# Kernel optimization log

Measured on AMD Instinct MI355X. Metric: run time of the kernel, lower is better.

The kernel has to match this reference:

```python
import jax, jax.numpy as jnp
import numpy as np

# Hyperparameters from init_kwargs
K = 1024           # num_embeddings
D = 256            # embedding_dim
COMMIT = 0.25      # commitment_cost
DECAY = 0.99
LAMBDA = 1e-05
NU = 0.1
TAU = 0.5


def setup_inputs() -> dict:
    key = jax.random.key(0)
    k1, k2, k3 = jax.random.split(key, 3)
    B, H, W = 32, 32, 32
    N = B * H * W
    inputs = jax.random.normal(k1, (B, D, H, W), jnp.float32)
    weight = jax.random.normal(k2, (K, D), jnp.float32) * 0.02  # codebook
    # EMA buffers as initialized on first training step (non-kmeans branch)
    ema_count = jnp.full((K,), N / K, jnp.float32)
    ema_weight = weight * ema_count[:, None]
    # Gumbel noise used by F.gumbel_softmax(-distances, tau, hard=True)
    gumbel_noise = jax.random.gumbel(k3, (N, K), jnp.float32)
    return {"inputs": inputs, "weight": weight, "ema_count": ema_count,
            "ema_weight": ema_weight, "gumbel_noise": gumbel_noise}


def reference(inputs, weight, ema_count, ema_weight, gumbel_noise):
    B, C, H, W = inputs.shape
    # b d h w -> (b h w) d
    x = jnp.transpose(inputs, (0, 2, 3, 1)).reshape(-1, C)  # [N, D]
    N = x.shape[0]

    distances = (jnp.sum(x * x, axis=1, keepdims=True)
                 + jnp.sum(weight * weight, axis=1)
                 - 2.0 * jnp.einsum('nd,kd->nk', x, weight))

    soft_encodings = jax.nn.softmax(-distances / TAU, axis=-1)  # [N, K]

    # Hard gumbel-softmax sample (computed under no_grad in torch):
    # argmax((logits + g)/tau) == argmax(logits + g), logits = -distances
    idx = jnp.argmax(-distances + gumbel_noise, axis=-1)        # [N]
    encodings = jax.nn.one_hot(idx, K, dtype=x.dtype)           # [N, K]

    quantized = (encodings @ weight).reshape(B, H, W, C)        # [B,H,W,D]

    # EMA codebook update (training branch, no_grad)
    new_count = ema_count * DECAY + jnp.sum(soft_encodings, axis=0) * (1.0 - DECAY)
    new_count = (new_count + LAMBDA) / (N + K * LAMBDA) * N
    d_weight = jnp.einsum('nk,nd->kd', soft_encodings, x)
    new_ema_weight = ema_weight * DECAY + d_weight * (1.0 - DECAY)
    new_embedding = new_ema_weight / new_count[:, None]

    # Negative-entropy commitment loss on soft assignments
    probs = soft_encodings
    loss_latents = jnp.mean(jnp.sum(probs * jnp.log(jnp.clip(probs, 1e-08)), axis=-1))
    loss = COMMIT * loss_latents

    # quantized + nu*(quantized - detach(quantized)) == quantized in value
    quantized = quantized + NU * (quantized - jax.lax.stop_gradient(quantized))

    avg_probs = jnp.mean(encodings, axis=0)
    perplexity = jnp.exp(-jnp.sum(avg_probs * jnp.log(avg_probs + 1e-10)))

    quantized_out = jnp.transpose(quantized, (0, 3, 1, 2))  # [B,D,H,W]
    return (loss, quantized_out, perplexity, encodings,
            new_count, new_ema_weight, new_embedding)
```

## Files before the change

### kernel.cpp

```cpp
#include <hip/hip_runtime.h>
#include <math.h>

#define NROWS 32768
#define KCB   1024
#define DDIM  256
#define NHALF 16384

#define O_LOSS 0
#define O_Q    1
#define O_PERP 8388609
#define O_ENC  8388610
#define O_NCNT 41943042
#define O_EMAW 41944066
#define O_EMB  42206210

#define E_XS3   2
#define E_S     12582914

#define W_WSQ  0
#define W_XSQ  1024
#define W_IDX  33792
#define W_COL  66560
#define W_HCNT 67584
#define W_BENT 68608
#define W_T2I  77824
#define W_WB   143360
#define W_MROW 274432
#define W_IROW 307200

typedef __attribute__((ext_vector_type(8))) short bf16x8;
typedef __attribute__((ext_vector_type(4))) float f32x4;

#define GLOAD_LDS16(g, l) __builtin_amdgcn_global_load_lds( \
    (const __attribute__((address_space(1))) unsigned int*)(g), \
    (__attribute__((address_space(3))) unsigned int*)(l), 16, 0, 0)

__device__ __forceinline__ float wred_sum(float v) {
#pragma unroll
  for (int off = 32; off > 0; off >>= 1) v += __shfl_xor(v, off);
  return v;
}
__device__ __forceinline__ ushort f2bf(float f) {
  union { float f; unsigned u; } c; c.f = f;
  unsigned u = c.u;
  return (ushort)((u + 0x7fffu + ((u >> 16) & 1u)) >> 16);
}
__device__ __forceinline__ float bf2f(ushort h) {
  union { unsigned u; float f; } c; c.u = ((unsigned)h) << 16;
  return c.f;
}

__global__ void k_init(float* __restrict__ hcnt, float* __restrict__ colsum) {
  int i = blockIdx.x * 256 + threadIdx.x;
  if (i < 1024) { hcnt[i] = 0.f; colsum[i] = 0.f; }
}

__global__ void k_wsplit(const float* __restrict__ w, float* __restrict__ wsq,
                         ushort* __restrict__ WB) {
  int t = threadIdx.x;
  int lane = t & 63, wv = t >> 6;
  int k = blockIdx.x * 4 + wv;
  int d0 = lane * 4;
  float4 v = *(const float4*)&w[(size_t)k * DDIM + d0];
  float s = v.x * v.x + v.y * v.y + v.z * v.z + v.w * v.w;
  s = wred_sum(s);
  if (lane == 0) wsq[k] = s;
  float vv[4] = {v.x, v.y, v.z, v.w};
  union { ushort u[4]; uint2 q; } hh;
#pragma unroll
  for (int q = 0; q < 4; ++q) hh.u[q] = f2bf(vv[q]);
  *(uint2*)&WB[(size_t)k * 256 + d0] = hh.q;
}

__global__ __launch_bounds__(256) void k_xsplit(const float* __restrict__ x,
                                                ushort* __restrict__ XS3,
                                                float* __restrict__ xsq) {
  __shared__ __align__(16) ushort sl[32 * 776];
  __shared__ float sq[32 * 9];
  int t = threadIdx.x;
  int b = blockIdx.x >> 5, mt = blockIdx.x & 31;
  int m0 = mt * 32, mloc = t & 31, dgrp = t >> 5;
  const float* xb = x + (size_t)b * DDIM * 1024 + m0 + mloc;
  float s = 0.f;
#pragma unroll
  for (int jj = 0; jj < 8; ++jj) {
    int d0 = dgrp * 32 + jj * 4;
    float vv[4];
#pragma unroll
    for (int q = 0; q < 4; ++q) vv[q] = xb[(size_t)(d0 + q) * 1024];
    union { ushort u[4]; uint2 q; } hh, mi, lo;
#pragma unroll
    for (int q = 0; q < 4; ++q) {
      float v = vv[q];
      ushort h = f2bf(v);
      float r1 = v - bf2f(h);
      ushort m_ = f2bf(r1);
      float r2 = r1 - bf2f(m_);
      hh.u[q] = h; mi.u[q] = m_; lo.u[q] = f2bf(r2);
      s = fmaf(v, v, s);
    }
    int base = mloc * 776;
    *(uint2*)&sl[base + d0] = hh.q;
    *(uint2*)&sl[base + 256 + d0] = mi.q;
    *(uint2*)&sl[base + 512 + d0] = lo.q;
  }
  sq[mloc * 9 + dgrp] = s;
  __syncthreads();
  if (t < 32) {
    float ss = 0.f;
#pragma unroll
    for (int gq = 0; gq < 8; ++gq) ss += sq[t * 9 + gq];
    xsq[b * 1024 + m0 + t] = ss;
  }
  ushort* dst = XS3 + (size_t)(b * 1024 + m0) * 768;
#pragma unroll
  for (int p = 0; p < 12; ++p) {
    int idx = p * 256 + t;
    int row = idx / 96;
    int co = idx - row * 96;
    *(uint4*)&dst[(size_t)row * 768 + co * 8] = *(uint4*)&sl[row * 776 + co * 8];
  }
}

__global__ __launch_bounds__(256) void k_gemm1t(const ushort* __restrict__ XS3h,
                                                const ushort* __restrict__ WB,
                                                const float* __restrict__ wsq,
                                                const float* __restrict__ xsqh,
                                                float* __restrict__ S) {
  __shared__ __align__(16) ushort Asl[2][8192];
  __shared__ __align__(16) ushort Bsl[2][8192];
  __shared__ float xsl[128];
  __shared__ float wsl[128];
  int t = threadIdx.x;
  int h = blockIdx.x;
  int xcd = h & 7, seq = h >> 3;
  int kt = seq & 7;
  int nt = xcd * 16 + (seq >> 3);
  int n0 = nt * 128;
  int k0 = kt * 128;
  int l = t & 63, wid = t >> 6;
  int wr = wid >> 1, wc = wid & 1;
  int hi = l >> 4, c = l & 15;

  if (t < 128) { xsl[t] = xsqh[n0 + t]; wsl[t] = wsq[k0 + t]; }

  f32x4 zero = {0.f, 0.f, 0.f, 0.f};
  f32x4 acc[4][4];
#pragma unroll
  for (int i = 0; i < 4; ++i)
#pragma unroll
    for (int j = 0; j < 4; ++j) acc[i][j] = zero;

  const char* XSb = (const char*)XS3h;
  const char* WBb = (const char*)WB;
  int lr = l >> 3;
  int lsw = ((l & 7) ^ lr) << 4;

#define STAGE(s_, b_)                                                              \
  {                                                                                \
    size_t bofs_ = (size_t)((s_) & 3) << 7;                                        \
    size_t aofs_ = ((s_) < 4) ? ((size_t)(s_) << 7)                                \
                              : (size_t)(512 + (((s_) - 4) << 7));                 \
    char* Ad_ = (char*)Asl + (b_) * 16384;                                         \
    char* Bd_ = (char*)Bsl + (b_) * 16384;                                         \
    _Pragma("unroll")                                                              \
    for (int q_ = 0; q_ < 4; ++q_) {                                               \
      int seg_ = wid * 32 + q_ * 8;                                                \
      GLOAD_LDS16(XSb + (size_t)(n0 + seg_ + lr) * 1536 + aofs_ + lsw,             \
                  Ad_ + seg_ * 128);                                               \
      GLOAD_LDS16(WBb + (size_t)(k0 + seg_ + lr) * 512 + bofs_ + lsw,              \
                  Bd_ + seg_ * 128);                                               \
    }                                                                              \
  }

  STAGE(0, 0);
  asm volatile("s_waitcnt vmcnt(0)" ::: "memory");
  __builtin_amdgcn_s_barrier();
  __builtin_amdgcn_sched_barrier(0);

  int buf = 0;
  for (int s = 0; s < 8; ++s) {
    if (s < 7) STAGE(s + 1, buf ^ 1);
    const ushort* Ab = &Asl[buf][0];
    const ushort* Bb = &Bsl[buf][0];
#pragma unroll
    for (int kk = 0; kk < 2; ++kk) {
      bf16x8 af[4], bg[4];
#pragma unroll
      for (int i = 0; i < 4; ++i) {
        int row = wr * 64 + i * 16 + c;
        int ch = (kk * 4 + hi) ^ (row & 7);
        af[i] = *(const bf16x8*)&Ab[row * 64 + ch * 8];
      }
#pragma unroll
      for (int j = 0; j < 4; ++j) {
        int row = wc * 64 + j * 16 + c;
        int ch = (kk * 4 + hi) ^ (row & 7);
        bg[j] = *(const bf16x8*)&Bb[row * 64 + ch * 8];
      }
#pragma unroll
      for (int i = 0; i < 4; ++i)
#pragma unroll
        for (int j = 0; j < 4; ++j)
          acc[i][j] = __builtin_amdgcn_mfma_f32_16x16x32_bf16(af[i], bg[j], acc[i][j], 0, 0, 0);
    }
    asm volatile("s_waitcnt vmcnt(0)" ::: "memory");
    __builtin_amdgcn_s_barrier();
    buf ^= 1;
  }
#undef STAGE

#pragma unroll
  for (int i = 0; i < 4; ++i) {
#pragma unroll
    for (int r = 0; r < 4; ++r) {
      int nl = wr * 64 + i * 16 + hi * 4 + r;
      float xs = xsl[nl];
#pragma unroll
      for (int j = 0; j < 4; ++j) {
        int kl = wc * 64 + j * 16 + c;
        float nd = fmaf(2.f, acc[i][j][r], -(xs + wsl[kl]));
        S[(size_t)(n0 + nl) * 1024 + k0 + kl] = nd;
      }
    }
  }
}

__global__ __launch_bounds__(512) void k_rowfuse(const float* __restrict__ S,
                                                 const float* __restrict__ Gh,
                                                 float* __restrict__ benth,
                                                 int* __restrict__ t2igh,
                                                 ushort* __restrict__ sTp) {
  __shared__ ushort lds[64 * 65];
  __shared__ float Ml[64], Il[64];
  __shared__ float went[8];
  int t = threadIdx.x;
  int l = t & 63, wv = t >> 6;
  int n0 = blockIdx.x * 64;
  float entacc = 0.f;
  for (int it = 0; it < 8; ++it) {
    int nloc = wv * 8 + it;
    int n = n0 + nloc;
    const float* row = S + ((size_t)n << 10);
    const float* grow = Gh + ((size_t)n << 10);
    float v[16];
    float mx = -3.0e38f;
    float v1 = -3.0e38f, v2 = -3.0e38f;
    int i1 = 0x7fffffff, i2 = 0x7fffffff;
#pragma unroll
    for (int j = 0; j < 4; ++j) {
      float4 a = *(const float4*)&row[j * 256 + l * 4];
      float4 gg = *(const float4*)&grow[j * 256 + l * 4];
      float av[4] = {a.x, a.y, a.z, a.w};
      float gv[4] = {gg.x, gg.y, gg.z, gg.w};
#pragma unroll
      for (int q = 0; q < 4; ++q) {
        v[j * 4 + q] = av[q];
        mx = fmaxf(mx, av[q]);
        float sc = av[q] + gv[q];
        int kk = j * 256 + l * 4 + q;
        if (sc > v1 || (sc == v1 && kk < i1)) { v2 = v1; i2 = i1; v1 = sc; i1 = kk; }
        else if (sc > v2 || (sc == v2 && kk < i2)) { v2 = sc; i2 = kk; }
      }
    }
#pragma unroll
    for (int off = 1; off < 64; off <<= 1) {
      mx = fmaxf(mx, __shfl_xor(mx, off));
      float ov1 = __shfl_xor(v1, off), ov2 = __shfl_xor(v2, off);
      int oi1 = __shfl_xor(i1, off), oi2 = __shfl_xor(i2, off);
      bool fB = (ov1 > v1) || (ov1 == v1 && oi1 < i1);
      float nv1 = fB ? ov1 : v1; int ni1 = fB ? oi1 : i1;
      float ca = fB ? v1 : ov1;  int cia = fB ? i1 : oi1;
      float cb = fB ? ov2 : v2;  int cib = fB ? oi2 : i2;
      bool sB = (cb > ca) || (cb == ca && cib < cia);
      v1 = nv1; i1 = ni1;
      v2 = sB ? cb : ca; i2 = sB ? cib : cia;
    }
    float M = 2.f * mx;
    float e[16]; float ps = 0.f;
#pragma unroll
    for (int u = 0; u < 16; ++u) { e[u] = __expf(fmaf(2.f, v[u], -M)); ps += e[u]; }
    ps = wred_sum(ps);
    float inv = 1.f / ps;
    float ent = 0.f;
#pragma unroll
    for (int u = 0; u < 16; ++u) {
      float sfv = e[u] * inv;
      ent += sfv * __logf(fmaxf(sfv, 1e-8f));
    }
    ent = wred_sum(ent);
    entacc += ent;
    if (l == 0) {
      t2igh[n * 2] = i1; t2igh[n * 2 + 1] = i2;
      Ml[nloc] = M; Il[nloc] = inv;
    }
  }
  if (l == 0) went[wv] = entacc;
  __syncthreads();
  if (t == 0) {
    float s = 0.f;
#pragma unroll
    for (int q = 0; q < 8; ++q) s += went[q];
    benth[blockIdx.x] = s;
  }
  int row2 = t >> 3, c8 = (t & 7) * 8;
  float M2 = Ml[row2], inv2 = Il[row2];
  for (int kt = 0; kt < 16; ++kt) {
    int k0 = kt * 64;
    const float* sp = &S[(size_t)(n0 + row2) * 1024 + k0 + c8];
    float4 a = *(const float4*)sp;
    float4 b = *(const float4*)(sp + 4);
    float sv[8] = {a.x, a.y, a.z, a.w, b.x, b.y, b.z, b.w};
    ushort* d = &lds[row2 * 65 + c8];
#pragma unroll
    for (int j = 0; j < 8; ++j)
      d[j] = f2bf(__expf(fmaf(2.f, sv[j], -M2)) * inv2);
    __syncthreads();
    int krow = t >> 3, nc8 = (t & 7) * 8;
    uint* dst = (uint*)&sTp[(size_t)(k0 + krow) * NHALF + n0 + nc8];
#pragma unroll
    for (int j = 0; j < 4; ++j) {
      uint lo = lds[(nc8 + 2 * j) * 65 + krow];
      uint hh = lds[(nc8 + 2 * j + 1) * 65 + krow];
      dst[j] = lo | (hh << 16);
    }
    __syncthreads();
  }
}

__global__ __launch_bounds__(256) void k_rowstat(const float* __restrict__ S,
                                                 const float* __restrict__ Gh,
                                                 float* __restrict__ Mrowh,
                                                 float* __restrict__ Irowh,
                                                 float* __restrict__ benth,
                                                 int* __restrict__ t2igh) {
  __shared__ float went[4];
  int t = threadIdx.x;
  int l = t & 63, wv = t >> 6;
  int n = blockIdx.x * 4 + wv;
  const float* row = S + ((size_t)n << 10);
  const float* grow = Gh + ((size_t)n << 10);
  float v[16];
  float mx = -3.0e38f;
  float v1 = -3.0e38f, v2 = -3.0e38f;
  int i1 = 0x7fffffff, i2 = 0x7fffffff;
#pragma unroll
  for (int j = 0; j < 4; ++j) {
    float4 a = *(const float4*)&row[j * 256 + l * 4];
    float4 gg = *(const float4*)&grow[j * 256 + l * 4];
    float av[4] = {a.x, a.y, a.z, a.w};
    float gv[4] = {gg.x, gg.y, gg.z, gg.w};
#pragma unroll
    for (int q = 0; q < 4; ++q) {
      v[j * 4 + q] = av[q];
      mx = fmaxf(mx, av[q]);
      float sc = av[q] + gv[q];
      int kk = j * 256 + l * 4 + q;
      if (sc > v1 || (sc == v1 && kk < i1)) { v2 = v1; i2 = i1; v1 = sc; i1 = kk; }
      else if (sc > v2 || (sc == v2 && kk < i2)) { v2 = sc; i2 = kk; }
    }
  }
#pragma unroll
  for (int off = 1; off < 64; off <<= 1) {
    mx = fmaxf(mx, __shfl_xor(mx, off));
    float ov1 = __shfl_xor(v1, off), ov2 = __shfl_xor(v2, off);
    int oi1 = __shfl_xor(i1, off), oi2 = __shfl_xor(i2, off);
    bool fB = (ov1 > v1) || (ov1 == v1 && oi1 < i1);
    float nv1 = fB ? ov1 : v1; int ni1 = fB ? oi1 : i1;
    float ca = fB ? v1 : ov1;  int cia = fB ? i1 : oi1;
    float cb = fB ? ov2 : v2;  int cib = fB ? oi2 : i2;
    bool sB = (cb > ca) || (cb == ca && cib < cia);
    v1 = nv1; i1 = ni1;
    v2 = sB ? cb : ca; i2 = sB ? cib : cia;
  }
  float M = 2.f * mx;
  float e[16]; float ps = 0.f;
#pragma unroll
  for (int u = 0; u < 16; ++u) { e[u] = __expf(fmaf(2.f, v[u], -M)); ps += e[u]; }
  ps = wred_sum(ps);
  float inv = 1.f / ps;
  float ent = 0.f;
#pragma unroll
  for (int u = 0; u < 16; ++u) {
    float sfv = e[u] * inv;
    ent += sfv * __logf(fmaxf(sfv, 1e-8f));
  }
  ent = wred_sum(ent);
  if (l == 0) {
    t2igh[n * 2] = i1; t2igh[n * 2 + 1] = i2;
    Mrowh[n] = M; Irowh[n] = inv;
    went[wv] = ent;
  }
  __syncthreads();
  if (t == 0) benth[blockIdx.x] = went[0] + went[1] + went[2] + went[3];
}

__global__ __launch_bounds__(512) void k_rowwrite(const float* __restrict__ S,
                                                  const float* __restrict__ Mrowh,
                                                  const float* __restrict__ Irowh,
                                                  ushort* __restrict__ sTp) {
  __shared__ ushort lds[64 * 65];
  __shared__ float Ml[64], Il[64];
  int t = threadIdx.x;
  int n0 = blockIdx.x * 64;
  if (t < 64) { Ml[t] = Mrowh[n0 + t]; Il[t] = Irowh[n0 + t]; }
  __syncthreads();
  for (int kt = 0; kt < 16; ++kt) {
    int k0 = kt * 64;
    int row = t >> 3, c8 = (t & 7) * 8;
    float M = Ml[row], inv = Il[row];
    const float* sp = &S[(size_t)(n0 + row) * 1024 + k0 + c8];
    float4 a = *(const float4*)sp;
    float4 b = *(const float4*)(sp + 4);
    float sv[8] = {a.x, a.y, a.z, a.w, b.x, b.y, b.z, b.w};
    ushort* d = &lds[row * 65 + c8];
#pragma unroll
    for (int j = 0; j < 8; ++j)
      d[j] = f2bf(__expf(fmaf(2.f, sv[j], -M)) * inv);
    __syncthreads();
    int krow = t >> 3, nc8 = (t & 7) * 8;
    uint* dst = (uint*)&sTp[(size_t)(k0 + krow) * NHALF + n0 + nc8];
#pragma unroll
    for (int j = 0; j < 4; ++j) {
      uint lo = lds[(nc8 + 2 * j) * 65 + krow];
      uint hh = lds[(nc8 + 2 * j + 1) * 65 + krow];
      dst[j] = lo | (hh << 16);
    }
    __syncthreads();
  }
}

__global__ __launch_bounds__(256) void k_refine(const ushort* __restrict__ XS3,
                                                const float* __restrict__ w,
                                                const float* __restrict__ wsq,
                                                const float* __restrict__ xsq,
                                                const float* __restrict__ G,
                                                const int* __restrict__ t2ig,
                                                int* __restrict__ idxArr,
                                                float* __restrict__ hcnt) {
  int t = threadIdx.x;
  int l = t & 63, wv = t >> 6;
  int base = blockIdx.x * 64 + wv * 16;
  int d0 = l * 4;
  for (int rr = 0; rr < 16; ++rr) {
    int n = base + rr;
    const ushort* p = XS3 + (size_t)n * 768;
    union { uint2 q; ushort u[4]; } ha, ma, la;
    ha.q = *(const uint2*)&p[d0];
    ma.q = *(const uint2*)&p[256 + d0];
    la.q = *(const uint2*)&p[512 + d0];
    float xv[4];
#pragma unroll
    for (int q = 0; q < 4; ++q) xv[q] = bf2f(ha.u[q]) + bf2f(ma.u[q]) + bf2f(la.u[q]);
    float xs = xsq[n];
    int ia = t2ig[n * 2], ib = t2ig[n * 2 + 1];
    float sc[2];
    int ids[2] = {ia, ib};
#pragma unroll
    for (int cdd = 0; cdd < 2; ++cdd) {
      int id = ids[cdd];
      const float* wr = w + (size_t)id * DDIM;
      float4 wv4 = *(const float4*)&wr[d0];
      float d = xv[0] * wv4.x + xv[1] * wv4.y + xv[2] * wv4.z + xv[3] * wv4.w;
      d = wred_sum(d);
      sc[cdd] = fmaf(2.f, d, -xs) - wsq[id] + G[((size_t)n << 10) + id];
    }
    int win = (sc[1] > sc[0] || (sc[1] == sc[0] && ib < ia)) ? ib : ia;
    if (l == 0) {
      idxArr[n] = win;
      atomicAdd(&hcnt[win], 1.f);
    }
  }
}

__global__ void k_quant(const float* __restrict__ w, const int* __restrict__ idxArr,
                        float* __restrict__ outQ) {
  int n = blockIdx.x * 256 + threadIdx.x;
  int b = n >> 10, m = n & 1023;
  int id = idxArr[n];
  const float* wr = w + (size_t)id * DDIM;
  float* o = outQ + (size_t)b * DDIM * 1024 + m;
#pragma unroll 4
  for (int d = 0; d < DDIM; ++d) o[(size_t)d * 1024] = wr[d];
}

__global__ __launch_bounds__(512) void k_gemm2_mfma(const ushort* __restrict__ sT0,
                                                    const ushort* __restrict__ sT1,
                                                    const float* __restrict__ x,
                                                    ushort* __restrict__ P,
                                                    float* __restrict__ colsum) {
  __shared__ __align__(16) ushort Abuf[256 * 72];
  __shared__ __align__(16) ushort Bbuf[128 * 72];
  int t = threadIdx.x;
  int h = blockIdx.x;
  int xcd = h & 7, seq = h >> 3;
  int ns = xcd * 4 + (seq >> 3);
  int ktdt = seq & 7;
  int kt = ktdt & 3, dt = ktdt >> 2;
  int k0 = kt * 256, d0 = dt * 128;
  int l = t & 63, wv = t >> 6;
  int wk = wv >> 1, wd = wv & 1;
  const ushort* Abase = (ns < 16) ? sT0 : sT1;
  size_t nloc0 = (size_t)(ns & 15) * 1024;
  f32x4 zero = {0.f, 0.f, 0.f, 0.f};
  f32x4 acc[4][4];
#pragma unroll
  for (int i = 0; i < 4; ++i)
#pragma unroll
    for (int j = 0; j < 4; ++j) acc[i][j] = zero;
  float colacc[4] = {0.f, 0.f, 0.f, 0.f};

  int colv = (t & 7) * 8;
  int rbase = t >> 3;
  for (int s = 0; s < 16; ++s) {
#pragma unroll
    for (int p = 0; p < 4; ++p) {
      int row = p * 64 + rbase;
      const uint* ap = (const uint*)(Abase + (size_t)(k0 + row) * NHALF + nloc0 + s * 64 + colv);
      uint4 v; v.x = ap[0]; v.y = ap[1]; v.z = ap[2]; v.w = ap[3];
      *(uint4*)&Abuf[row * 72 + colv] = v;
    }
#pragma unroll
    for (int p = 0; p < 2; ++p) {
      int row = p * 64 + rbase;
      const float* xp = &x[((size_t)ns * DDIM + d0 + row) * 1024 + s * 64 + colv];
      float4 a = *(const float4*)xp;
      float4 b = *(const float4*)(xp + 4);
      union { ushort u[8]; uint4 q; } pk;
      pk.u[0] = f2bf(a.x); pk.u[1] = f2bf(a.y); pk.u[2] = f2bf(a.z); pk.u[3] = f2bf(a.w);
      pk.u[4] = f2bf(b.x); pk.u[5] = f2bf(b.y); pk.u[6] = f2bf(b.z); pk.u[7] = f2bf(b.w);
      *(uint4*)&Bbuf[row * 72 + colv] = pk.q;
    }
    __syncthreads();
    bf16x8 af[4], bfr[4];
#pragma unroll
    for (int nb2 = 0; nb2 < 2; ++nb2) {
#pragma unroll
      for (int sub = 0; sub < 4; ++sub) {
        af[sub] = *(const bf16x8*)&Abuf[(wk * 64 + sub * 16 + (l & 15)) * 72 + nb2 * 32 + (l >> 4) * 8];
        bfr[sub] = *(const bf16x8*)&Bbuf[(wd * 64 + sub * 16 + (l & 15)) * 72 + nb2 * 32 + (l >> 4) * 8];
      }
      if (dt == 0 && wd == 0) {
#pragma unroll
        for (int sub = 0; sub < 4; ++sub)
#pragma unroll
          for (int q = 0; q < 8; ++q)
            colacc[sub] += bf2f((ushort)af[sub][q]);
      }
#pragma unroll
      for (int i = 0; i < 4; ++i)
#pragma unroll
        for (int j = 0; j < 4; ++j)
          acc[i][j] = __builtin_amdgcn_mfma_f32_16x16x32_bf16(af[i], bfr[j], acc[i][j], 0, 0, 0);
    }
    __syncthreads();
  }
  ushort* Pb = P + (size_t)ns * (KCB * DDIM);
#pragma unroll
  for (int i = 0; i < 4; ++i)
#pragma unroll
    for (int j = 0; j < 4; ++j) {
#pragma unroll
      for (int r = 0; r < 4; ++r) {
        int k = k0 + wk * 64 + i * 16 + (l >> 4) * 4 + r;
        int d = d0 + wd * 64 + j * 16 + (l & 15);
        Pb[(size_t)k * DDIM + d] = f2bf(acc[i][j][r]);
      }
    }
  if (dt == 0 && wd == 0) {
#pragma unroll
    for (int sub = 0; sub < 4; ++sub) {
      float s = colacc[sub];
      s += __shfl_xor(s, 16);
      s += __shfl_xor(s, 32);
      if (l < 16) atomicAdd(&colsum[k0 + wk * 64 + sub * 16 + l], s);
    }
  }
}

__global__ void k_final1(const float* __restrict__ hcnt, const float* __restrict__ bent,
                         float* __restrict__ out) {
  __shared__ float red[1024];
  int t = threadIdx.x;
  float s = 0.f;
  for (int i = t; i < 4352; i += 1024) s += bent[i];
  red[t] = s;
  __syncthreads();
  for (int off = 512; off > 0; off >>= 1) { if (t < off) red[t] += red[t + off]; __syncthreads(); }
  if (t == 0) out[O_LOSS] = 0.25f * (red[0] / 32768.0f);
  __syncthreads();
  float avg = hcnt[t] * (1.0f / 32768.0f);
  red[t] = avg * logf(avg + 1e-10f);
  __syncthreads();
  for (int off = 512; off > 0; off >>= 1) { if (t < off) red[t] += red[t + off]; __syncthreads(); }
  if (t == 0) out[O_PERP] = expf(-red[0]);
}

__global__ void k_reduce_final2(const ushort* __restrict__ P,
                                const float* __restrict__ ema_w,
                                const float* __restrict__ ema_count,
                                const float* __restrict__ colsum,
                                float* __restrict__ outNC,
                                float* __restrict__ outEW,
                                float* __restrict__ outEMB) {
  int i4 = (blockIdx.x * 256 + threadIdx.x) * 4;
  int k = i4 >> 8;
  float nc = ema_count[k] * 0.99f + colsum[k] * 0.01f;
  nc = (nc + 1e-5f) / (32768.0f + 1024.0f * 1e-5f) * 32768.0f;
  if ((i4 & 255) == 0) outNC[k] = nc;
  float s0 = 0.f, s1 = 0.f, s2 = 0.f, s3 = 0.f;
#pragma unroll
  for (int ns = 0; ns < 32; ++ns) {
    uint2 v = *(const uint2*)&P[(size_t)ns * (KCB * DDIM) + i4];
    s0 += bf2f((ushort)(v.x & 0xffffu)); s1 += bf2f((ushort)(v.x >> 16));
    s2 += bf2f((ushort)(v.y & 0xffffu)); s3 += bf2f((ushort)(v.y >> 16));
  }
  float4 ew4 = *(const float4*)&ema_w[i4];
  float invnc = 1.0f / nc;
  float e0 = ew4.x * 0.99f + s0 * 0.01f;
  float e1 = ew4.y * 0.99f + s1 * 0.01f;
  float e2 = ew4.z * 0.99f + s2 * 0.01f;
  float e3 = ew4.w * 0.99f + s3 * 0.01f;
  float4 ewo = {e0, e1, e2, e3};
  float4 emo = {e0 * invnc, e1 * invnc, e2 * invnc, e3 * invnc};
  *(float4*)&outEW[i4] = ewo;
  *(float4*)&outEMB[i4] = emo;
}

__global__ void k_onehot(const int* __restrict__ idxArr, float* __restrict__ E) {
  int gid = blockIdx.x * 256 + threadIdx.x;
  int n = gid >> 8;
  int k4 = (gid & 255) * 4;
  int id = idxArr[n];
  float2* E2 = (float2*)E;
  size_t base = ((size_t)n * KCB + k4) >> 1;
  float2 vA = {(float)(k4 == id), (float)(k4 + 1 == id)};
  float2 vB = {(float)(k4 + 2 == id), (float)(k4 + 3 == id)};
  E2[base] = vA;
  E2[base + 1] = vB;
}

extern "C" void kernel_launch(void* const* d_in, const int* in_sizes, int n_in,
                              void* d_out, int out_size, void* d_ws, size_t ws_size,
                              hipStream_t stream) {
  const float* x = (const float*)d_in[0];
  const float* w = (const float*)d_in[1];
  const float* ema_count = (const float*)d_in[2];
  const float* ema_w = (const float*)d_in[3];
  const float* g = (const float*)d_in[4];
  float* out = (float*)d_out;
  float* ws = (float*)d_ws;

  float* wsq    = ws + W_WSQ;
  float* xsq    = ws + W_XSQ;
  int*   idxArr = (int*)(ws + W_IDX);
  float* colsum = ws + W_COL;
  float* hcnt   = ws + W_HCNT;
  float* bent   = ws + W_BENT;
  int*   top2i  = (int*)(ws + W_T2I);
  ushort* WB    = (ushort*)(ws + W_WB);
  float* Mrow   = ws + W_MROW;
  float* Irow   = ws + W_IROW;

  float* outQ = out + O_Q;
  float* outE = out + O_ENC;

  ushort* XS3    = (ushort*)(outE + E_XS3);
  float*  Sslot  = outE + E_S;
  ushort* Pbf    = (ushort*)Sslot;
  ushort* softT1 = (ushort*)(outE + E_XS3);
  ushort* softT0 = (ushort*)outQ;

  k_init<<<4, 256, 0, stream>>>(hcnt, colsum);
  k_wsplit<<<256, 256, 0, stream>>>(w, wsq, WB);
  k_xsplit<<<1024, 256, 0, stream>>>(x, XS3, xsq);
  k_gemm1t<<<1024, 256, 0, stream>>>(XS3, WB, wsq, xsq, Sslot);
  k_rowfuse<<<256, 512, 0, stream>>>(Sslot, g, bent, top2i, softT0);
  k_gemm1t<<<1024, 256, 0, stream>>>(XS3 + (size_t)NHALF * 768, WB,
                                     wsq, xsq + NHALF, Sslot);
  k_rowstat<<<4096, 256, 0, stream>>>(Sslot, g + (size_t)NHALF * 1024,
                                      Mrow, Irow, bent + 256, top2i + NHALF * 2);
  k_refine<<<512, 256, 0, stream>>>(XS3, w, wsq, xsq, g, top2i, idxArr, hcnt);
  k_rowwrite<<<256, 512, 0, stream>>>(Sslot, Mrow, Irow, softT1);
  k_gemm2_mfma<<<256, 512, 0, stream>>>(softT0, softT1, x, Pbf, colsum);
  k_reduce_final2<<<256, 256, 0, stream>>>(Pbf, ema_w, ema_count, colsum,
                                           out + O_NCNT, out + O_EMAW, out + O_EMB);
  k_final1<<<1, 1024, 0, stream>>>(hcnt, bent, out);
  k_quant<<<128, 256, 0, stream>>>(w, idxArr, outQ);
  k_onehot<<<32768, 256, 0, stream>>>(idxArr, outE);
}
```

Measured before the change: 324.4 us.

## Deepen GEMM1 prefetch to two stages and fold tiny init/final kernels

The distance GEMM main loop now keeps two stages of global-to-LDS loads in flight. It waits with a partial vmcnt instead of draining all loads each iteration, and issues stage s+2 after the compute barrier. Separately, the zero-init kernel is merged into k_wsplit and the loss/perplexity reduction is merged into block 0 of k_reduce_final2, which removes two launches. The deeper pipeline depends on the vmcnt(8) count exactly matching the per-stage load count. Folding the reduction into one block makes that block do extra serial work.

```diff
diff --git a/kernel.cpp b/kernel.cpp
--- a/kernel.cpp
+++ b/kernel.cpp
@@ -50,16 +50,15 @@
   return c.f;
 }
 
-__global__ void k_init(float* __restrict__ hcnt, float* __restrict__ colsum) {
-  int i = blockIdx.x * 256 + threadIdx.x;
-  if (i < 1024) { hcnt[i] = 0.f; colsum[i] = 0.f; }
-}
-
 __global__ void k_wsplit(const float* __restrict__ w, float* __restrict__ wsq,
-                         ushort* __restrict__ WB) {
-  int t = threadIdx.x;
+                         ushort* __restrict__ WB, float* __restrict__ hcnt,
+                         float* __restrict__ colsum) {
+  int t = threadIdx.x;
+  int b = blockIdx.x;
+  if (b < 4) hcnt[b * 256 + t] = 0.f;
+  else if (b < 8) colsum[(b - 4) * 256 + t] = 0.f;
   int lane = t & 63, wv = t >> 6;
-  int k = blockIdx.x * 4 + wv;
+  int k = b * 4 + wv;
   int d0 = lane * 4;
   float4 v = *(const float4*)&w[(size_t)k * DDIM + d0];
   float s = v.x * v.x + v.y * v.y + v.z * v.z + v.w * v.w;
@@ -174,13 +173,18 @@
   }
 
   STAGE(0, 0);
-  asm volatile("s_waitcnt vmcnt(0)" ::: "memory");
-  __builtin_amdgcn_s_barrier();
-  __builtin_amdgcn_sched_barrier(0);
+  STAGE(1, 1);
 
   int buf = 0;
+#pragma unroll 1
   for (int s = 0; s < 8; ++s) {
-    if (s < 7) STAGE(s + 1, buf ^ 1);
+    if (s < 7) {
+      asm volatile("s_waitcnt vmcnt(8)" ::: "memory");
+    } else {
+      asm volatile("s_waitcnt vmcnt(0)" ::: "memory");
+    }
+    __builtin_amdgcn_sched_barrier(0);
+    __builtin_amdgcn_s_barrier();
     const ushort* Ab = &Asl[buf][0];
     const ushort* Bb = &Bsl[buf][0];
 #pragma unroll
@@ -204,8 +208,8 @@
         for (int j = 0; j < 4; ++j)
           acc[i][j] = __builtin_amdgcn_mfma_f32_16x16x32_bf16(af[i], bg[j], acc[i][j], 0, 0, 0);
     }
-    asm volatile("s_waitcnt vmcnt(0)" ::: "memory");
     __builtin_amdgcn_s_barrier();
+    if (s < 6) STAGE(s + 2, buf);
     buf ^= 1;
   }
 #undef STAGE
@@ -578,36 +582,19 @@
   }
 }
 
-__global__ void k_final1(const float* __restrict__ hcnt, const float* __restrict__ bent,
-                         float* __restrict__ out) {
-  __shared__ float red[1024];
-  int t = threadIdx.x;
-  float s = 0.f;
-  for (int i = t; i < 4352; i += 1024) s += bent[i];
-  red[t] = s;
-  __syncthreads();
-  for (int off = 512; off > 0; off >>= 1) { if (t < off) red[t] += red[t + off]; __syncthreads(); }
-  if (t == 0) out[O_LOSS] = 0.25f * (red[0] / 32768.0f);
-  __syncthreads();
-  float avg = hcnt[t] * (1.0f / 32768.0f);
-  red[t] = avg * logf(avg + 1e-10f);
-  __syncthreads();
-  for (int off = 512; off > 0; off >>= 1) { if (t < off) red[t] += red[t + off]; __syncthreads(); }
-  if (t == 0) out[O_PERP] = expf(-red[0]);
-}
-
 __global__ void k_reduce_final2(const ushort* __restrict__ P,
                                 const float* __restrict__ ema_w,
                                 const float* __restrict__ ema_count,
                                 const float* __restrict__ colsum,
-                                float* __restrict__ outNC,
-                                float* __restrict__ outEW,
-                                float* __restrict__ outEMB) {
-  int i4 = (blockIdx.x * 256 + threadIdx.x) * 4;
+                                const float* __restrict__ hcnt,
+                                const float* __restrict__ bent,
+                                float* __restrict__ out) {
+  int t = threadIdx.x;
+  int i4 = (blockIdx.x * 256 + t) * 4;
   int k = i4 >> 8;
   float nc = ema_count[k] * 0.99f + colsum[k] * 0.01f;
   nc = (nc + 1e-5f) / (32768.0f + 1024.0f * 1e-5f) * 32768.0f;
-  if ((i4 & 255) == 0) outNC[k] = nc;
+  if ((i4 & 255) == 0) out[O_NCNT + k] = nc;
   float s0 = 0.f, s1 = 0.f, s2 = 0.f, s3 = 0.f;
 #pragma unroll
   for (int ns = 0; ns < 32; ++ns) {
@@ -623,8 +610,28 @@
   float e3 = ew4.w * 0.99f + s3 * 0.01f;
   float4 ewo = {e0, e1, e2, e3};
   float4 emo = {e0 * invnc, e1 * invnc, e2 * invnc, e3 * invnc};
-  *(float4*)&outEW[i4] = ewo;
-  *(float4*)&outEMB[i4] = emo;
+  *(float4*)&out[O_EMAW + i4] = ewo;
+  *(float4*)&out[O_EMB + i4] = emo;
+
+  if (blockIdx.x == 0) {
+    __shared__ float red[256];
+    float s = 0.f;
+    for (int i = t; i < 4352; i += 256) s += bent[i];
+    red[t] = s;
+    __syncthreads();
+    for (int off = 128; off > 0; off >>= 1) { if (t < off) red[t] += red[t + off]; __syncthreads(); }
+    if (t == 0) out[O_LOSS] = 0.25f * (red[0] / 32768.0f);
+    __syncthreads();
+    float pp = 0.f;
+    for (int i = t; i < 1024; i += 256) {
+      float avg = hcnt[i] * (1.0f / 32768.0f);
+      pp += avg * logf(avg + 1e-10f);
+    }
+    red[t] = pp;
+    __syncthreads();
+    for (int off = 128; off > 0; off >>= 1) { if (t < off) red[t] += red[t + off]; __syncthreads(); }
+    if (t == 0) out[O_PERP] = expf(-red[0]);
+  }
 }
 
 __global__ void k_onehot(const int* __restrict__ idxArr, float* __restrict__ E) {
@@ -671,8 +678,7 @@
   ushort* softT1 = (ushort*)(outE + E_XS3);
   ushort* softT0 = (ushort*)outQ;
 
-  k_init<<<4, 256, 0, stream>>>(hcnt, colsum);
-  k_wsplit<<<256, 256, 0, stream>>>(w, wsq, WB);
+  k_wsplit<<<256, 256, 0, stream>>>(w, wsq, WB, hcnt, colsum);
   k_xsplit<<<1024, 256, 0, stream>>>(x, XS3, xsq);
   k_gemm1t<<<1024, 256, 0, stream>>>(XS3, WB, wsq, xsq, Sslot);
   k_rowfuse<<<256, 512, 0, stream>>>(Sslot, g, bent, top2i, softT0);
@@ -683,9 +689,7 @@
   k_refine<<<512, 256, 0, stream>>>(XS3, w, wsq, xsq, g, top2i, idxArr, hcnt);
   k_rowwrite<<<256, 512, 0, stream>>>(Sslot, Mrow, Irow, softT1);
   k_gemm2_mfma<<<256, 512, 0, stream>>>(softT0, softT1, x, Pbf, colsum);
-  k_reduce_final2<<<256, 256, 0, stream>>>(Pbf, ema_w, ema_count, colsum,
-                                           out + O_NCNT, out + O_EMAW, out + O_EMB);
-  k_final1<<<1, 1024, 0, stream>>>(hcnt, bent, out);
+  k_reduce_final2<<<256, 256, 0, stream>>>(Pbf, ema_w, ema_count, colsum, hcnt, bent, out);
   k_quant<<<128, 256, 0, stream>>>(w, idxArr, outQ);
   k_onehot<<<32768, 256, 0, stream>>>(idxArr, outE);
 }
```

New measurement: 326.9 us. About the same (+0.8%).
